# Kernel optimization log

Hardware: AMD Instinct MI355X
Metric: run time of the kernel (lower is better)

Reference implementation:

```python
import jax, jax.numpy as jnp
import numpy as np

NLAYER = 3
EPS = 1e-5
NEG = -1e30  # stand-in for -inf in masked max


def _layernorm(h, g, b):
    mu = h.mean(-1, keepdims=True)
    v = ((h - mu) ** 2).mean(-1, keepdims=True)
    return (h - mu) * jax.lax.rsqrt(v + EPS) * g + b


def setup_inputs() -> dict:
    key = jax.random.key(0)
    ks = jax.random.split(key, 8)
    N, K, D = 8192, 8, 128
    s = 0.05
    x = jax.random.normal(ks[0], (N, D), jnp.float32)
    neigh = jax.random.randint(ks[1], (N, K), 0, N, dtype=jnp.int32)
    nbr_count = jax.random.randint(ks[2], (N,), 0, K + 1, dtype=jnp.int32)
    gcn_W = jax.random.normal(ks[3], (NLAYER, D, D), jnp.float32) * s
    gcn_b = jnp.zeros((NLAYER, D), jnp.float32)
    gcn_ln_g = jnp.ones((NLAYER, D), jnp.float32)
    gcn_ln_b = jnp.zeros((NLAYER, D), jnp.float32)
    sage_pool_W = jax.random.normal(ks[4], (D, D), jnp.float32) * s
    sage_pool_b = jnp.zeros((D,), jnp.float32)
    sage_merge_W = jax.random.normal(ks[5], (NLAYER, D, 2 * D), jnp.float32) * s
    sage_merge_b = jnp.zeros((NLAYER, D), jnp.float32)
    sage_ln_g = jnp.ones((NLAYER - 1, D), jnp.float32)
    sage_ln_b = jnp.zeros((NLAYER - 1, D), jnp.float32)
    return {"x": x, "neigh": neigh, "nbr_count": nbr_count,
            "gcn_W": gcn_W, "gcn_b": gcn_b, "gcn_ln_g": gcn_ln_g, "gcn_ln_b": gcn_ln_b,
            "sage_pool_W": sage_pool_W, "sage_pool_b": sage_pool_b,
            "sage_merge_W": sage_merge_W, "sage_merge_b": sage_merge_b,
            "sage_ln_g": sage_ln_g, "sage_ln_b": sage_ln_b}


def reference(x, neigh, nbr_count, gcn_W, gcn_b, gcn_ln_g, gcn_ln_b,
              sage_pool_W, sage_pool_b, sage_merge_W, sage_merge_b,
              sage_ln_g, sage_ln_b):
    N, D = x.shape
    K = neigh.shape[1]
    mask = jnp.arange(K)[None, :] < nbr_count[:, None]  # [N, K] valid neighbors

    # ---- GCN branch: dense symmetric-normalized adjacency with self loops ----
    rows = jnp.broadcast_to(jnp.arange(N)[:, None], neigh.shape)
    A = jnp.zeros((N, N), x.dtype).at[rows, neigh].add(mask.astype(x.dtype))
    A = jnp.minimum(A, 1.0)  # dedupe multi-edges (original sets 1.0)
    A = A.at[jnp.arange(N), jnp.arange(N)].set(1.0)  # self loop (node[0] in list)
    dinv = jax.lax.rsqrt(A.sum(-1))  # degree^-0.5, >= 1 due to self loop
    Ah = dinv[:, None] * A * dinv[None, :]

    h = x
    first = None
    for i in range(NLAYER):
        nxt = h @ gcn_W[i].T + gcn_b[i]
        if i == 0:
            first = nxt
        nxt = jax.nn.relu(Ah @ nxt)
        # residual=True: layer 1 adds first-layer pre-prop enc, later layers add h
        h = _layernorm(nxt + (first if i == 0 else h), gcn_ln_g[i], gcn_ln_b[i])
    gcn_out = h

    # ---- SAGE branch: max-pool over children (self excluded), concat, merge ----
    def pool(node_encs):
        g = jnp.where(mask[:, :, None], node_encs[neigh], NEG)  # [N, K, D]
        p = g.max(axis=1)
        return jnp.where((nbr_count > 0)[:, None], p, 0.0)  # leaf -> zeros

    ne1 = jax.nn.relu(x @ sage_pool_W.T + sage_pool_b)  # pool linear only layer 1
    s = jax.nn.relu(jnp.concatenate([x, pool(ne1)], -1) @ sage_merge_W[0].T + sage_merge_b[0])
    for i in range(1, NLAYER):
        nxt = jax.nn.relu(jnp.concatenate([s, pool(s)], -1) @ sage_merge_W[i].T + sage_merge_b[i])
        s = _layernorm(nxt + s, sage_ln_g[i - 1], sage_ln_b[i - 1])

    return jnp.concatenate([gcn_out, s], -1)  # [N, 2*treehid]
```

## Files before the change

kernel.cpp:

```cpp
#include <hip/hip_runtime.h>

#define NND 8192
#define KNBR 8
#define DD 128
#define EPSF 1e-5f
#define TSH 16384

typedef __attribute__((ext_vector_type(8))) short bf16x8;
typedef __attribute__((ext_vector_type(4))) float f32x4;

__device__ __forceinline__ unsigned short f2bf(float f) {
    unsigned u = __float_as_uint(f);
    u += 0x7FFF + ((u >> 16) & 1);
    return (unsigned short)(u >> 16);
}

__device__ __forceinline__ float bf_lo(unsigned u) { return __uint_as_float(u << 16); }
__device__ __forceinline__ float bf_hi(unsigned u) { return __uint_as_float(u & 0xFFFF0000u); }
__device__ __forceinline__ float bfs(unsigned short u) {
    return __uint_as_float((unsigned)u << 16);
}

__device__ __forceinline__ bf16x8 cvt8(const float* __restrict__ p) {
    float4 lo = *(const float4*)p;
    float4 hi = *(const float4*)(p + 4);
    bf16x8 r;
    r[0] = f2bf(lo.x); r[1] = f2bf(lo.y); r[2] = f2bf(lo.z); r[3] = f2bf(lo.w);
    r[4] = f2bf(hi.x); r[5] = f2bf(hi.y); r[6] = f2bf(hi.z); r[7] = f2bf(hi.w);
    return r;
}

__device__ __forceinline__ void gload_lds16(const unsigned short* g, unsigned short* l) {
    __builtin_amdgcn_global_load_lds(
        (const __attribute__((address_space(1))) unsigned int*)(g),
        (__attribute__((address_space(3))) unsigned int*)(l), 16, 0, 0);
}

__device__ __forceinline__ void stage1(unsigned short* sh, const unsigned short* wb, int tid) {
    int lane = tid & 63, w = tid >> 6;
#pragma unroll
    for (int r = 0; r < 8; ++r) {
        int blk = (r * 4 + w) * 512;
        gload_lds16(wb + blk + lane * 8, sh + blk);
    }
}

__device__ __forceinline__ void stage_cvt_sw(unsigned short* sh, const float* __restrict__ W,
                                             int wstr, int tid) {
    int r = tid >> 1, h = tid & 1;
    const float* src = W + (size_t)r * wstr;
#pragma unroll
    for (int i = 0; i < 8; ++i) {
        int ch = h * 8 + i;
        *(bf16x8*)(sh + r * 128 + ((ch ^ (r & 7)) << 3)) = cvt8(src + ch * 8);
    }
}

__device__ __forceinline__ void load_af(bf16x8* af, const unsigned short* __restrict__ A,
                                        int rowBase, int lane) {
    int idx = lane & 15, q = lane >> 4;
    const unsigned short* Ar = A + (size_t)(rowBase + idx) * DD;
#pragma unroll
    for (int s = 0; s < 4; ++s) af[s] = *(const bf16x8*)(Ar + s * 32 + q * 8);
}

__device__ __forceinline__ void load_af_f32(bf16x8* af, const float* __restrict__ A,
                                            int rowBase, int lane) {
    int idx = lane & 15, q = lane >> 4;
    const float* Ar = A + (size_t)(rowBase + idx) * DD;
#pragma unroll
    for (int s = 0; s < 4; ++s) af[s] = cvt8(Ar + s * 32 + q * 8);
}

__device__ __forceinline__ void mma_sw(const bf16x8* af, const unsigned short* shB,
                                       int lane, f32x4* acc) {
    int idx = lane & 15, q = lane >> 4, k7 = idx & 7;
#pragma unroll
    for (int s = 0; s < 4; ++s)
#pragma unroll
        for (int ct = 0; ct < 8; ++ct) {
            int ch = (4 * s + q) ^ k7;
            bf16x8 bf = *(const bf16x8*)(shB + (ct * 16 + idx) * 128 + ch * 8);
            acc[ct] = __builtin_amdgcn_mfma_f32_16x16x32_bf16(af[s], bf, acc[ct], 0, 0, 0);
        }
}

__device__ __forceinline__ void store_fw_b16(unsigned short* __restrict__ out,
        int rowBase, int lane, const f32x4* acc, const float* __restrict__ bias, bool relu) {
    int idx = lane & 15, q = lane >> 4;
#pragma unroll
    for (int ct = 0; ct < 8; ++ct) {
        float b = bias[ct * 16 + idx];
#pragma unroll
        for (int r = 0; r < 4; ++r) {
            float v = acc[ct][r] + b;
            if (relu) v = fmaxf(v, 0.f);
            out[(size_t)(rowBase + q * 4 + r) * DD + ct * 16 + idx] = f2bf(v);
        }
    }
}

__device__ __forceinline__ void lnstore_fw_br(float* __restrict__ outF, int ostride, int oOff,
        const unsigned short* __restrict__ residB, int rowBase, int lane, f32x4* acc,
        const float* __restrict__ bias, const float* __restrict__ g,
        const float* __restrict__ bv, unsigned short* __restrict__ outB) {
    int idx = lane & 15, q = lane >> 4;
    float rsum[4] = {0.f, 0.f, 0.f, 0.f};
#pragma unroll
    for (int ct = 0; ct < 8; ++ct) {
        float b = bias[ct * 16 + idx];
#pragma unroll
        for (int r = 0; r < 4; ++r) {
            float t = fmaxf(acc[ct][r] + b, 0.f)
                    + bfs(residB[(size_t)(rowBase + q * 4 + r) * DD + ct * 16 + idx]);
            acc[ct][r] = t;
            rsum[r] += t;
        }
    }
#pragma unroll
    for (int r = 0; r < 4; ++r)
#pragma unroll
        for (int m = 1; m < 16; m <<= 1) rsum[r] += __shfl_xor(rsum[r], m, 64);
    float mu[4];
#pragma unroll
    for (int r = 0; r < 4; ++r) mu[r] = rsum[r] * (1.f / 128.f);
    float var[4] = {0.f, 0.f, 0.f, 0.f};
#pragma unroll
    for (int ct = 0; ct < 8; ++ct)
#pragma unroll
        for (int r = 0; r < 4; ++r) {
            float d = acc[ct][r] - mu[r];
            var[r] += d * d;
        }
#pragma unroll
    for (int r = 0; r < 4; ++r)
#pragma unroll
        for (int m = 1; m < 16; m <<= 1) var[r] += __shfl_xor(var[r], m, 64);
    float rs[4];
#pragma unroll
    for (int r = 0; r < 4; ++r) rs[r] = rsqrtf(var[r] * (1.f / 128.f) + EPSF);
#pragma unroll
    for (int ct = 0; ct < 8; ++ct) {
        float gg = g[ct * 16 + idx], bb = bv[ct * 16 + idx];
#pragma unroll
        for (int r = 0; r < 4; ++r) {
            float o = (acc[ct][r] - mu[r]) * rs[r] * gg + bb;
            size_t row = (size_t)(rowBase + q * 4 + r);
            if (outF) outF[row * ostride + oOff + ct * 16 + idx] = o;
            if (outB) outB[row * DD + ct * 16 + idx] = f2bf(o);
        }
    }
}

__device__ __forceinline__ float wave_sum(float s) {
#pragma unroll
    for (int m = 1; m < 64; m <<= 1) s += __shfl_xor(s, m, 64);
    return s;
}

__device__ __forceinline__ void prop_pool_row(int row, int lane,
        const unsigned short* __restrict__ nxtB, const unsigned short* __restrict__ residB,
        const unsigned short* __restrict__ enc,
        const float* __restrict__ dinv, const int* __restrict__ kept,
        const int* __restrict__ neigh, const int* __restrict__ cnt,
        const float* __restrict__ g, const float* __restrict__ b,
        float* __restrict__ outF, int oStride,
        unsigned short* __restrict__ outB, unsigned short* __restrict__ P) {
    const unsigned* nxt2 = (const unsigned*)nxtB;
    const unsigned* e32  = (const unsigned*)enc;
    int nb[KNBR];
#pragma unroll
    for (int j = 0; j < KNBR; ++j) nb[j] = neigh[row * KNBR + j];
    int km = kept[row];
    int c  = cnt[row];
    float di = dinv[row];
    int idxs[KNBR]; float wj[KNBR];
#pragma unroll
    for (int j = 0; j < KNBR; ++j) {
        bool k = (km >> j) & 1;
        idxs[j] = k ? nb[j] : row;
        wj[j] = k ? dinv[nb[j]] : 0.f;
    }
    unsigned vv[KNBR], pv[KNBR];
#pragma unroll
    for (int j = 0; j < KNBR; ++j) vv[j] = nxt2[(size_t)idxs[j] * 64 + lane];
#pragma unroll
    for (int j = 0; j < KNBR; ++j) {
        int src = (j < c) ? nb[j] : row;
        pv[j] = e32[(size_t)src * 64 + lane];
    }
    unsigned su = nxt2[(size_t)row * 64 + lane];
    unsigned ru = ((const unsigned*)residB)[(size_t)row * 64 + lane];
    float ax = di * bf_lo(su), ay = di * bf_hi(su);
#pragma unroll
    for (int j = 0; j < KNBR; ++j) {
        ax = fmaf(wj[j], bf_lo(vv[j]), ax);
        ay = fmaf(wj[j], bf_hi(vv[j]), ay);
    }
    float vx = fmaxf(di * ax, 0.f) + bf_lo(ru);
    float vy = fmaxf(di * ay, 0.f) + bf_hi(ru);
    float mu = wave_sum(vx + vy) * (1.f / 128.f);
    float dx = vx - mu, dy = vy - mu;
    float var = wave_sum(dx * dx + dy * dy) * (1.f / 128.f);
    float rs = rsqrtf(var + EPSF);
    float2 gg = ((const float2*)g)[lane];
    float2 bb = ((const float2*)b)[lane];
    float ox = dx * rs * gg.x + bb.x;
    float oy = dy * rs * gg.y + bb.y;
    if (outF) {
        float2 o; o.x = ox; o.y = oy;
        *reinterpret_cast<float2*>(outF + (size_t)row * oStride + lane * 2) = o;
    }
    if (outB) {
        unsigned pk = (unsigned)f2bf(ox) | ((unsigned)f2bf(oy) << 16);
        *(unsigned*)(outB + (size_t)row * DD + lane * 2) = pk;
    }
    float px = -1e30f, py = -1e30f;
#pragma unroll
    for (int j = 0; j < KNBR; ++j) {
        if (j < c) {
            px = fmaxf(px, bf_lo(pv[j]));
            py = fmaxf(py, bf_hi(pv[j]));
        }
    }
    unsigned o = 0u;
    if (c > 0)
        o = (__float_as_uint(px) >> 16) | (__float_as_uint(py) & 0xFFFF0000u);
    ((unsigned*)P)[(size_t)row * 64 + lane] = o;
}

__global__ __launch_bounds__(256)
void mega_all(const float* __restrict__ x,
              const float* __restrict__ gcnW, const float* __restrict__ poolW,
              const float* __restrict__ mW,
              const float* __restrict__ gB0, const float* __restrict__ pB,
              const float* __restrict__ mB0,
              const int* __restrict__ neigh, const int* __restrict__ cnt,
              float* __restrict__ dinv, int* __restrict__ kept,
              unsigned short* __restrict__ wbuf,
              unsigned short* __restrict__ Gb, unsigned short* __restrict__ E1b,
              unsigned short* __restrict__ S1pb) {
    __shared__ __align__(16) unsigned short shB[TSH];
    const int bid = blockIdx.x, tid = threadIdx.x;
    const int lane = tid & 63, w = tid >> 6;

    if (bid < 384) {
        int grp = bid >> 7, bx = bid & 127;
        const float* W; int str;
        if (grp == 0)      { W = gcnW;  str = 128; }
        else if (grp == 1) { W = poolW; str = 128; }
        else               { W = mW;    str = 256; }
        stage_cvt_sw(shB, W, str, tid);
        int rowBase = (bx * 4 + w) * 16;
        bf16x8 af[4];
        load_af_f32(af, x, rowBase, lane);
        __syncthreads();
        f32x4 acc[8];
#pragma unroll
        for (int i = 0; i < 8; ++i) acc[i] = (f32x4){0.f, 0.f, 0.f, 0.f};
        mma_sw(af, shB, lane, acc);
        if (grp == 0)      store_fw_b16(Gb, rowBase, lane, acc, gB0, false);
        else if (grp == 1) store_fw_b16(E1b, rowBase, lane, acc, pB, true);
        else               store_fw_b16(S1pb, rowBase, lane, acc, mB0, false);
    } else if (bid < 416) {
        int i = (bid - 384) * 256 + tid;
        int c = cnt[i];
        int nb[KNBR];
#pragma unroll
        for (int j = 0; j < KNBR; ++j) nb[j] = neigh[i * KNBR + j];
        int mask = 0, deg = 1;
#pragma unroll
        for (int j = 0; j < KNBR; ++j) {
            if (j < c) {
                int v = nb[j];
                bool dup = (v == i);
                for (int jj = 0; jj < j; ++jj)
                    if (nb[jj] == v) { dup = true; }
                if (!dup) { mask |= (1 << j); deg++; }
            }
        }
        dinv[i] = rsqrtf((float)deg);
        kept[i] = mask;
    } else {
        int cid = (bid - 416) * 256 + tid;
        int u = cid >> 11, c2 = cid & 2047, row = c2 >> 4, ch = c2 & 15;
        const float* base; int str; int t;
        if (u == 0)      { t = 1; base = gcnW + 16384;       str = 128; }
        else if (u == 1) { t = 2; base = gcnW + 32768;       str = 128; }
        else if (u == 2) { t = 5; base = mW + 128;           str = 256; }
        else if (u == 3) { t = 6; base = mW + 32768;         str = 256; }
        else if (u == 4) { t = 7; base = mW + 32768 + 128;   str = 256; }
        else if (u == 5) { t = 8; base = mW + 65536;         str = 256; }
        else             { t = 9; base = mW + 65536 + 128;   str = 256; }
        bf16x8 v = cvt8(base + (size_t)row * str + ch * 8);
        *(bf16x8*)(wbuf + t * TSH + row * 128 + ((ch ^ (row & 7)) << 3)) = v;
    }
}

__global__ __launch_bounds__(256)
void prop_pool(const unsigned short* __restrict__ nxtB,
               const unsigned short* __restrict__ residB,
               const float* __restrict__ dinv, const int* __restrict__ kept,
               const int* __restrict__ neigh, const int* __restrict__ cnt,
               const float* __restrict__ g, const float* __restrict__ b,
               float* __restrict__ outF, int oStride,
               unsigned short* __restrict__ outB,
               const unsigned short* __restrict__ enc,
               unsigned short* __restrict__ P) {
    int row = blockIdx.x * 4 + (threadIdx.x >> 6);
    int lane = threadIdx.x & 63;
    prop_pool_row(row, lane, nxtB, residB, enc, dinv, kept, neigh, cnt,
                  g, b, outF, oStride, outB, P);
}

__global__ __launch_bounds__(256)
void gemm_step4(const unsigned short* __restrict__ Pb, const unsigned short* __restrict__ H1b,
                const unsigned short* __restrict__ wbuf, const float* __restrict__ gB1,
                const unsigned short* __restrict__ S1pb, unsigned short* __restrict__ S1b,
                unsigned short* __restrict__ Gb) {
    __shared__ __align__(16) unsigned short shB[TSH];
    const int tid = threadIdx.x, lane = tid & 63, w = tid >> 6;
    const int rowBase = ((int)blockIdx.x * 4 + w) * 16;
    f32x4 acc[8];
#pragma unroll
    for (int i = 0; i < 8; ++i) acc[i] = (f32x4){0.f, 0.f, 0.f, 0.f};
    bf16x8 af[4];
    if (blockIdx.y == 0) {
        stage1(shB, wbuf + 5 * TSH, tid);
        load_af(af, Pb, rowBase, lane);
        __syncthreads();
        mma_sw(af, shB, lane, acc);
        int idx = lane & 15, q = lane >> 4;
#pragma unroll
        for (int ct = 0; ct < 8; ++ct)
#pragma unroll
            for (int r = 0; r < 4; ++r) {
                size_t o = (size_t)(rowBase + q * 4 + r) * DD + ct * 16 + idx;
                float v = fmaxf(bfs(S1pb[o]) + acc[ct][r], 0.f);
                S1b[o] = f2bf(v);
            }
    } else {
        stage1(shB, wbuf + 1 * TSH, tid);
        load_af(af, H1b, rowBase, lane);
        __syncthreads();
        mma_sw(af, shB, lane, acc);
        store_fw_b16(Gb, rowBase, lane, acc, gB1, false);
    }
}

__global__ __launch_bounds__(256)
void gemm_step6(const unsigned short* __restrict__ S1b, const unsigned short* __restrict__ Pb,
                const unsigned short* __restrict__ H2b,
                const unsigned short* __restrict__ wbuf,
                const float* __restrict__ mB1, const float* __restrict__ gB2,
                const float* __restrict__ sg, const float* __restrict__ sb,
                unsigned short* __restrict__ S2b, unsigned short* __restrict__ Gb) {
    __shared__ __align__(16) unsigned short shB[2 * TSH];
    const int tid = threadIdx.x, lane = tid & 63, w = tid >> 6;
    const int rowBase = ((int)blockIdx.x * 4 + w) * 16;
    f32x4 acc[8];
#pragma unroll
    for (int i = 0; i < 8; ++i) acc[i] = (f32x4){0.f, 0.f, 0.f, 0.f};
    if (blockIdx.y == 0) {
        stage1(shB, wbuf + 6 * TSH, tid);
        stage1(shB + TSH, wbuf + 7 * TSH, tid);
        bf16x8 af1[4], af2[4];
        load_af(af1, S1b, rowBase, lane);
        load_af(af2, Pb, rowBase, lane);
        __syncthreads();
        mma_sw(af1, shB, lane, acc);
        mma_sw(af2, shB + TSH, lane, acc);
        lnstore_fw_br(nullptr, DD, 0, S1b, rowBase, lane, acc, mB1, sg, sb, S2b);
    } else {
        stage1(shB, wbuf + 2 * TSH, tid);
        bf16x8 af[4];
        load_af(af, H2b, rowBase, lane);
        __syncthreads();
        mma_sw(af, shB, lane, acc);
        store_fw_b16(Gb, rowBase, lane, acc, gB2, false);
    }
}

__global__ __launch_bounds__(256)
void gemm_final(const unsigned short* __restrict__ S2b, const unsigned short* __restrict__ Pb,
                const unsigned short* __restrict__ wbuf,
                const float* __restrict__ mB2,
                const float* __restrict__ sg2, const float* __restrict__ sb2,
                float* __restrict__ out) {
    __shared__ __align__(16) unsigned short shB[2 * TSH];
    const int tid = threadIdx.x, lane = tid & 63, w = tid >> 6;
    const int rowBase = ((int)blockIdx.x * 4 + w) * 16;
    f32x4 acc[8];
#pragma unroll
    for (int i = 0; i < 8; ++i) acc[i] = (f32x4){0.f, 0.f, 0.f, 0.f};
    stage1(shB, wbuf + 8 * TSH, tid);
    stage1(shB + TSH, wbuf + 9 * TSH, tid);
    bf16x8 af1[4], af2[4];
    load_af(af1, S2b, rowBase, lane);
    load_af(af2, Pb, rowBase, lane);
    __syncthreads();
    mma_sw(af1, shB, lane, acc);
    mma_sw(af2, shB + TSH, lane, acc);
    lnstore_fw_br(out, 2 * DD, DD, S2b, rowBase, lane, acc, mB2, sg2, sb2, nullptr);
}

extern "C" void kernel_launch(void* const* d_in, const int* in_sizes, int n_in,
                              void* d_out, int out_size, void* d_ws, size_t ws_size,
                              hipStream_t stream) {
    (void)in_sizes; (void)n_in; (void)out_size; (void)ws_size;
    const float* x      = (const float*)d_in[0];
    const int*   neigh  = (const int*)d_in[1];
    const int*   cnt    = (const int*)d_in[2];
    const float* gcnW   = (const float*)d_in[3];
    const float* gcnB   = (const float*)d_in[4];
    const float* gcnG   = (const float*)d_in[5];
    const float* gcnBb  = (const float*)d_in[6];
    const float* poolW  = (const float*)d_in[7];
    const float* poolB  = (const float*)d_in[8];
    const float* mW     = (const float*)d_in[9];
    const float* mB     = (const float*)d_in[10];
    const float* sg     = (const float*)d_in[11];
    const float* sb     = (const float*)d_in[12];
    float* out = (float*)d_out;

    char* ws = (char*)d_ws;
    float* dinv = (float*)ws;
    int*   kept = (int*)(ws + 32 * 1024);
    unsigned short* wbuf = (unsigned short*)(ws + 64 * 1024);
    unsigned short* Gb   = (unsigned short*)(ws + 448 * 1024);
    unsigned short* E1b  = Gb   + NND * DD;
    unsigned short* S1pb = E1b  + NND * DD;
    unsigned short* Pb   = S1pb + NND * DD;
    unsigned short* H1b  = Pb   + NND * DD;
    unsigned short* H2b  = H1b  + NND * DD;
    unsigned short* S1b  = H2b  + NND * DD;
    unsigned short* S2b  = S1b  + NND * DD;

    dim3 blk(256);
    dim3 rgrid(NND / 4);

    mega_all<<<dim3(472), blk, 0, stream>>>(x, gcnW, poolW, mW, gcnB, poolB, mB,
                                            neigh, cnt, dinv, kept, wbuf,
                                            Gb, E1b, S1pb);
    prop_pool<<<rgrid, blk, 0, stream>>>(Gb, Gb, dinv, kept, neigh, cnt,
                                         gcnG, gcnBb, nullptr, DD, H1b, E1b, Pb);
    gemm_step4<<<dim3(128, 2), blk, 0, stream>>>(Pb, H1b, wbuf, gcnB + DD,
                                                 S1pb, S1b, Gb);
    prop_pool<<<rgrid, blk, 0, stream>>>(Gb, H1b, dinv, kept, neigh, cnt,
                                         gcnG + DD, gcnBb + DD, nullptr, DD,
                                         H2b, S1b, Pb);
    gemm_step6<<<dim3(128, 2), blk, 0, stream>>>(S1b, Pb, H2b, wbuf,
                                                 mB + DD, gcnB + 2 * DD, sg, sb,
                                                 S2b, Gb);
    prop_pool<<<rgrid, blk, 0, stream>>>(Gb, H2b, dinv, kept, neigh, cnt,
                                         gcnG + 2 * DD, gcnBb + 2 * DD,
                                         out, 2 * DD, nullptr, S2b, Pb);
    gemm_final<<<dim3(128), blk, 0, stream>>>(S2b, Pb, wbuf, mB + 2 * DD,
                                              sg + DD, sb + DD, out);
}
```

Measured before the change: 129.3 us.

## Split GEMM blocks by output column halves and K-split final merge GEMM

The non-LayerNorm GEMMs are split into two blocks per row tile, each computing 64 output columns from a half-size staged weight tile, which doubles grid size and halves LDS use per block. The final merge GEMM now assigns the two K halves (S2 and pooled) to different waves over 32 rows and reduces the partial sums through shared memory before LayerNorm. This aims to raise occupancy and parallelism on the 256-CU device for these small GEMMs. In exchange, activation A-fragments are loaded twice, there is more redundant staging, and the final kernel gains an extra barrier and an LDS exchange.

```diff
diff --git a/kernel.cpp b/kernel.cpp
--- a/kernel.cpp
+++ b/kernel.cpp
@@ -5,6 +5,8 @@
 #define DD 128
 #define EPSF 1e-5f
 #define TSH 16384
+#define HSH 8192
+#define XSTR 132
 
 typedef __attribute__((ext_vector_type(8))) short bf16x8;
 typedef __attribute__((ext_vector_type(4))) float f32x4;
@@ -45,13 +47,22 @@
     }
 }
 
-__device__ __forceinline__ void stage_cvt_sw(unsigned short* sh, const float* __restrict__ W,
-                                             int wstr, int tid) {
-    int r = tid >> 1, h = tid & 1;
-    const float* src = W + (size_t)r * wstr;
-#pragma unroll
-    for (int i = 0; i < 8; ++i) {
-        int ch = h * 8 + i;
+__device__ __forceinline__ void stage_half(unsigned short* sh, const unsigned short* wb, int tid) {
+    int lane = tid & 63, w = tid >> 6;
+#pragma unroll
+    for (int r = 0; r < 4; ++r) {
+        int blk = (r * 4 + w) * 512;
+        gload_lds16(wb + blk + lane * 8, sh + blk);
+    }
+}
+
+__device__ __forceinline__ void stage_cvt_sw_h(unsigned short* sh, const float* __restrict__ W,
+                                               int wstr, int rowOff, int tid) {
+    int r = tid >> 2, qtr = tid & 3;
+    const float* src = W + (size_t)(rowOff + r) * wstr;
+#pragma unroll
+    for (int i = 0; i < 4; ++i) {
+        int ch = qtr * 4 + i;
         *(bf16x8*)(sh + r * 128 + ((ch ^ (r & 7)) << 3)) = cvt8(src + ch * 8);
     }
 }
@@ -85,17 +96,31 @@
         }
 }
 
-__device__ __forceinline__ void store_fw_b16(unsigned short* __restrict__ out,
-        int rowBase, int lane, const f32x4* acc, const float* __restrict__ bias, bool relu) {
+__device__ __forceinline__ void mma_sw4(const bf16x8* af, const unsigned short* shB,
+                                        int lane, f32x4* acc) {
+    int idx = lane & 15, q = lane >> 4, k7 = idx & 7;
+#pragma unroll
+    for (int s = 0; s < 4; ++s)
+#pragma unroll
+        for (int ct = 0; ct < 4; ++ct) {
+            int ch = (4 * s + q) ^ k7;
+            bf16x8 bf = *(const bf16x8*)(shB + (ct * 16 + idx) * 128 + ch * 8);
+            acc[ct] = __builtin_amdgcn_mfma_f32_16x16x32_bf16(af[s], bf, acc[ct], 0, 0, 0);
+        }
+}
+
+__device__ __forceinline__ void store_h_b16(unsigned short* __restrict__ out,
+        int rowBase, int colBase, int lane, const f32x4* acc,
+        const float* __restrict__ bias, bool relu) {
     int idx = lane & 15, q = lane >> 4;
 #pragma unroll
-    for (int ct = 0; ct < 8; ++ct) {
-        float b = bias[ct * 16 + idx];
+    for (int ct = 0; ct < 4; ++ct) {
+        float b = bias[colBase + ct * 16 + idx];
 #pragma unroll
         for (int r = 0; r < 4; ++r) {
             float v = acc[ct][r] + b;
             if (relu) v = fmaxf(v, 0.f);
-            out[(size_t)(rowBase + q * 4 + r) * DD + ct * 16 + idx] = f2bf(v);
+            out[(size_t)(rowBase + q * 4 + r) * DD + colBase + ct * 16 + idx] = f2bf(v);
         }
     }
 }
@@ -240,30 +265,31 @@
               unsigned short* __restrict__ wbuf,
               unsigned short* __restrict__ Gb, unsigned short* __restrict__ E1b,
               unsigned short* __restrict__ S1pb) {
-    __shared__ __align__(16) unsigned short shB[TSH];
+    __shared__ __align__(16) unsigned short shB[HSH];
     const int bid = blockIdx.x, tid = threadIdx.x;
     const int lane = tid & 63, w = tid >> 6;
 
-    if (bid < 384) {
-        int grp = bid >> 7, bx = bid & 127;
+    if (bid < 768) {
+        int grp = bid >> 8, sub = bid & 255;
+        int bx = sub >> 1, colHalf = sub & 1, colBase = colHalf * 64;
         const float* W; int str;
         if (grp == 0)      { W = gcnW;  str = 128; }
         else if (grp == 1) { W = poolW; str = 128; }
         else               { W = mW;    str = 256; }
-        stage_cvt_sw(shB, W, str, tid);
+        stage_cvt_sw_h(shB, W, str, colBase, tid);
         int rowBase = (bx * 4 + w) * 16;
         bf16x8 af[4];
         load_af_f32(af, x, rowBase, lane);
         __syncthreads();
-        f32x4 acc[8];
-#pragma unroll
-        for (int i = 0; i < 8; ++i) acc[i] = (f32x4){0.f, 0.f, 0.f, 0.f};
-        mma_sw(af, shB, lane, acc);
-        if (grp == 0)      store_fw_b16(Gb, rowBase, lane, acc, gB0, false);
-        else if (grp == 1) store_fw_b16(E1b, rowBase, lane, acc, pB, true);
-        else               store_fw_b16(S1pb, rowBase, lane, acc, mB0, false);
-    } else if (bid < 416) {
-        int i = (bid - 384) * 256 + tid;
+        f32x4 acc[4];
+#pragma unroll
+        for (int i = 0; i < 4; ++i) acc[i] = (f32x4){0.f, 0.f, 0.f, 0.f};
+        mma_sw4(af, shB, lane, acc);
+        if (grp == 0)      store_h_b16(Gb, rowBase, colBase, lane, acc, gB0, false);
+        else if (grp == 1) store_h_b16(E1b, rowBase, colBase, lane, acc, pB, true);
+        else               store_h_b16(S1pb, rowBase, colBase, lane, acc, mB0, false);
+    } else if (bid < 800) {
+        int i = (bid - 768) * 256 + tid;
         int c = cnt[i];
         int nb[KNBR];
 #pragma unroll
@@ -282,7 +308,7 @@
         dinv[i] = rsqrtf((float)deg);
         kept[i] = mask;
     } else {
-        int cid = (bid - 416) * 256 + tid;
+        int cid = (bid - 800) * 256 + tid;
         int u = cid >> 11, c2 = cid & 2047, row = c2 >> 4, ch = c2 & 15;
         const float* base; int str; int t;
         if (u == 0)      { t = 1; base = gcnW + 16384;       str = 128; }
@@ -318,33 +344,35 @@
                 const unsigned short* __restrict__ wbuf, const float* __restrict__ gB1,
                 const unsigned short* __restrict__ S1pb, unsigned short* __restrict__ S1b,
                 unsigned short* __restrict__ Gb) {
-    __shared__ __align__(16) unsigned short shB[TSH];
+    __shared__ __align__(16) unsigned short shB[HSH];
     const int tid = threadIdx.x, lane = tid & 63, w = tid >> 6;
-    const int rowBase = ((int)blockIdx.x * 4 + w) * 16;
-    f32x4 acc[8];
-#pragma unroll
-    for (int i = 0; i < 8; ++i) acc[i] = (f32x4){0.f, 0.f, 0.f, 0.f};
+    const int bx = (int)blockIdx.x >> 1, colHalf = blockIdx.x & 1;
+    const int colBase = colHalf * 64;
+    const int rowBase = (bx * 4 + w) * 16;
+    f32x4 acc[4];
+#pragma unroll
+    for (int i = 0; i < 4; ++i) acc[i] = (f32x4){0.f, 0.f, 0.f, 0.f};
     bf16x8 af[4];
     if (blockIdx.y == 0) {
-        stage1(shB, wbuf + 5 * TSH, tid);
+        stage_half(shB, wbuf + 5 * TSH + colHalf * HSH, tid);
         load_af(af, Pb, rowBase, lane);
         __syncthreads();
-        mma_sw(af, shB, lane, acc);
+        mma_sw4(af, shB, lane, acc);
         int idx = lane & 15, q = lane >> 4;
 #pragma unroll
-        for (int ct = 0; ct < 8; ++ct)
+        for (int ct = 0; ct < 4; ++ct)
 #pragma unroll
             for (int r = 0; r < 4; ++r) {
-                size_t o = (size_t)(rowBase + q * 4 + r) * DD + ct * 16 + idx;
+                size_t o = (size_t)(rowBase + q * 4 + r) * DD + colBase + ct * 16 + idx;
                 float v = fmaxf(bfs(S1pb[o]) + acc[ct][r], 0.f);
                 S1b[o] = f2bf(v);
             }
     } else {
-        stage1(shB, wbuf + 1 * TSH, tid);
+        stage_half(shB, wbuf + 1 * TSH + colHalf * HSH, tid);
         load_af(af, H1b, rowBase, lane);
         __syncthreads();
-        mma_sw(af, shB, lane, acc);
-        store_fw_b16(Gb, rowBase, lane, acc, gB1, false);
+        mma_sw4(af, shB, lane, acc);
+        store_h_b16(Gb, rowBase, colBase, lane, acc, gB1, false);
     }
 }
 
@@ -356,12 +384,12 @@
                 const float* __restrict__ sg, const float* __restrict__ sb,
                 unsigned short* __restrict__ S2b, unsigned short* __restrict__ Gb) {
     __shared__ __align__(16) unsigned short shB[2 * TSH];
-    const int tid = threadIdx.x, lane = tid & 63, w = tid >> 6;
-    const int rowBase = ((int)blockIdx.x * 4 + w) * 16;
-    f32x4 acc[8];
-#pragma unroll
-    for (int i = 0; i < 8; ++i) acc[i] = (f32x4){0.f, 0.f, 0.f, 0.f};
-    if (blockIdx.y == 0) {
+    const int bid = blockIdx.x, tid = threadIdx.x, lane = tid & 63, w = tid >> 6;
+    if (bid < 128) {
+        const int rowBase = (bid * 4 + w) * 16;
+        f32x4 acc[8];
+#pragma unroll
+        for (int i = 0; i < 8; ++i) acc[i] = (f32x4){0.f, 0.f, 0.f, 0.f};
         stage1(shB, wbuf + 6 * TSH, tid);
         stage1(shB + TSH, wbuf + 7 * TSH, tid);
         bf16x8 af1[4], af2[4];
@@ -372,12 +400,18 @@
         mma_sw(af2, shB + TSH, lane, acc);
         lnstore_fw_br(nullptr, DD, 0, S1b, rowBase, lane, acc, mB1, sg, sb, S2b);
     } else {
-        stage1(shB, wbuf + 2 * TSH, tid);
+        int sub = bid - 128;
+        int bx = sub >> 1, colHalf = sub & 1, colBase = colHalf * 64;
+        const int rowBase = (bx * 4 + w) * 16;
+        f32x4 acc[4];
+#pragma unroll
+        for (int i = 0; i < 4; ++i) acc[i] = (f32x4){0.f, 0.f, 0.f, 0.f};
+        stage_half(shB, wbuf + 2 * TSH + colHalf * HSH, tid);
         bf16x8 af[4];
         load_af(af, H2b, rowBase, lane);
         __syncthreads();
-        mma_sw(af, shB, lane, acc);
-        store_fw_b16(Gb, rowBase, lane, acc, gB2, false);
+        mma_sw4(af, shB, lane, acc);
+        store_h_b16(Gb, rowBase, colBase, lane, acc, gB2, false);
     }
 }
 
@@ -388,20 +422,36 @@
                 const float* __restrict__ sg2, const float* __restrict__ sb2,
                 float* __restrict__ out) {
     __shared__ __align__(16) unsigned short shB[2 * TSH];
+    __shared__ float xch[32 * XSTR];
     const int tid = threadIdx.x, lane = tid & 63, w = tid >> 6;
-    const int rowBase = ((int)blockIdx.x * 4 + w) * 16;
-    f32x4 acc[8];
-#pragma unroll
-    for (int i = 0; i < 8; ++i) acc[i] = (f32x4){0.f, 0.f, 0.f, 0.f};
     stage1(shB, wbuf + 8 * TSH, tid);
     stage1(shB + TSH, wbuf + 9 * TSH, tid);
-    bf16x8 af1[4], af2[4];
-    load_af(af1, S2b, rowBase, lane);
-    load_af(af2, Pb, rowBase, lane);
+    const int rt = w & 1, unit = w >> 1;
+    const int rowBase = (int)blockIdx.x * 32 + rt * 16;
+    bf16x8 af[4];
+    load_af(af, unit ? Pb : S2b, rowBase, lane);
     __syncthreads();
-    mma_sw(af1, shB, lane, acc);
-    mma_sw(af2, shB + TSH, lane, acc);
-    lnstore_fw_br(out, 2 * DD, DD, S2b, rowBase, lane, acc, mB2, sg2, sb2, nullptr);
+    f32x4 acc[8];
+#pragma unroll
+    for (int i = 0; i < 8; ++i) acc[i] = (f32x4){0.f, 0.f, 0.f, 0.f};
+    mma_sw(af, shB + unit * TSH, lane, acc);
+    int idx = lane & 15, q = lane >> 4;
+    if (unit) {
+#pragma unroll
+        for (int ct = 0; ct < 8; ++ct)
+#pragma unroll
+            for (int r = 0; r < 4; ++r)
+                xch[(rt * 16 + q * 4 + r) * XSTR + ct * 16 + idx] = acc[ct][r];
+    }
+    __syncthreads();
+    if (!unit) {
+#pragma unroll
+        for (int ct = 0; ct < 8; ++ct)
+#pragma unroll
+            for (int r = 0; r < 4; ++r)
+                acc[ct][r] += xch[(rt * 16 + q * 4 + r) * XSTR + ct * 16 + idx];
+        lnstore_fw_br(out, 2 * DD, DD, S2b, rowBase, lane, acc, mB2, sg2, sb2, nullptr);
+    }
 }
 
 extern "C" void kernel_launch(void* const* d_in, const int* in_sizes, int n_in,
@@ -439,22 +489,22 @@
     dim3 blk(256);
     dim3 rgrid(NND / 4);
 
-    mega_all<<<dim3(472), blk, 0, stream>>>(x, gcnW, poolW, mW, gcnB, poolB, mB,
+    mega_all<<<dim3(856), blk, 0, stream>>>(x, gcnW, poolW, mW, gcnB, poolB, mB,
                                             neigh, cnt, dinv, kept, wbuf,
                                             Gb, E1b, S1pb);
     prop_pool<<<rgrid, blk, 0, stream>>>(Gb, Gb, dinv, kept, neigh, cnt,
                                          gcnG, gcnBb, nullptr, DD, H1b, E1b, Pb);
-    gemm_step4<<<dim3(128, 2), blk, 0, stream>>>(Pb, H1b, wbuf, gcnB + DD,
+    gemm_step4<<<dim3(256, 2), blk, 0, stream>>>(Pb, H1b, wbuf, gcnB + DD,
                                                  S1pb, S1b, Gb);
     prop_pool<<<rgrid, blk, 0, stream>>>(Gb, H1b, dinv, kept, neigh, cnt,
                                          gcnG + DD, gcnBb + DD, nullptr, DD,
                                          H2b, S1b, Pb);
-    gemm_step6<<<dim3(128, 2), blk, 0, stream>>>(S1b, Pb, H2b, wbuf,
-                                                 mB + DD, gcnB + 2 * DD, sg, sb,
-                                                 S2b, Gb);
+    gemm_step6<<<dim3(384), blk, 0, stream>>>(S1b, Pb, H2b, wbuf,
+                                              mB + DD, gcnB + 2 * DD, sg, sb,
+                                              S2b, Gb);
     prop_pool<<<rgrid, blk, 0, stream>>>(Gb, H2b, dinv, kept, neigh, cnt,
                                          gcnG + 2 * DD, gcnBb + 2 * DD,
                                          out, 2 * DD, nullptr, S2b, Pb);
-    gemm_final<<<dim3(128), blk, 0, stream>>>(S2b, Pb, wbuf, mB + 2 * DD,
+    gemm_final<<<dim3(256), blk, 0, stream>>>(S2b, Pb, wbuf, mB + 2 * DD,
                                               sg + DD, sb + DD, out);
 }
```

Measured after the change: 129.1 us. Within noise of the previous version (-0.1%).
